# Performance work log

Measured on AMD Instinct MI355X. Metric: run time of the kernel, lower is better.

## Reference

```python
import jax, jax.numpy as jnp
import numpy as np

B, T, D, H, C = 256, 512, 64, 512, 1

def setup_inputs() -> dict:
    key = jax.random.key(0)
    ks = jax.random.split(key, 12)
    return {
        "x": jax.random.normal(ks[0], (B, T, D), jnp.float32),
        "w_ih_mu": jax.random.normal(ks[1], (D, 4 * H), jnp.float32) * 0.1,
        "w_ih_rho": jax.random.normal(ks[2], (D, 4 * H), jnp.float32) - 6.0,
        "eps_ih": jax.random.normal(ks[3], (D, 4 * H), jnp.float32),
        "w_hh_mu": jax.random.normal(ks[4], (H, 4 * H), jnp.float32) * 0.1,
        "w_hh_rho": jax.random.normal(ks[5], (H, 4 * H), jnp.float32) - 6.0,
        "eps_hh": jax.random.normal(ks[6], (H, 4 * H), jnp.float32),
        "b_mu": jax.random.normal(ks[7], (4 * H,), jnp.float32) * 0.1,
        "b_rho": jax.random.normal(ks[8], (4 * H,), jnp.float32) - 6.0,
        "eps_b": jax.random.normal(ks[9], (4 * H,), jnp.float32),
        "lin_w": jax.random.normal(ks[10], (C, H), jnp.float32) * 0.04,
        "lin_b": jax.random.normal(ks[11], (C,), jnp.float32) * 0.04,
    }

def _sample(mu, rho, eps):
    # blitz reparameterization: sigma = log1p(exp(rho))
    return mu + jnp.log1p(jnp.exp(rho)) * eps

def reference(x, w_ih_mu, w_ih_rho, eps_ih, w_hh_mu, w_hh_rho, eps_hh,
              b_mu, b_rho, eps_b, lin_w, lin_b):
    w_ih = _sample(w_ih_mu, w_ih_rho, eps_ih)
    w_hh = _sample(w_hh_mu, w_hh_rho, eps_hh)
    b = _sample(b_mu, b_rho, eps_b)

    # precompute input projections for all timesteps: [T, B, 4H]
    x_proj = jnp.einsum('btd,dg->tbg', x, w_ih) + b

    def step(carry, xp_t):
        h, c = carry
        gates = xp_t + h @ w_hh                      # [B, 4H]
        i, f, g, o = jnp.split(gates, 4, axis=-1)
        i = jax.nn.sigmoid(i)
        f = jax.nn.sigmoid(f)
        g = jnp.tanh(g)
        o = jax.nn.sigmoid(o)
        c = f * c + i * g
        h = o * jnp.tanh(c)
        return (h, c), None

    h0 = jnp.zeros((x.shape[0], w_hh.shape[0]), x.dtype)
    (h_last, _), _ = jax.lax.scan(step, (h0, h0), x_proj)
    # original takes outputs[:, -1, :] == last hidden state, then Linear
    return h_last @ lin_w.T + lin_b
```

## Files before the change

### kernel.cpp

```cpp
#include <hip/hip_runtime.h>

typedef unsigned short u16;
typedef unsigned long long u64;
typedef short v8s __attribute__((ext_vector_type(8)));
typedef float v4f __attribute__((ext_vector_type(4)));
typedef unsigned v2u __attribute__((ext_vector_type(2)));
typedef unsigned v4u __attribute__((ext_vector_type(4)));

#define Bb 256
#define Tt 512
#define Dd 64
#define Hh 512
#define G4 2048

#define NGROUP 16
#define NCHUNK 16
#define BT 16
#define HC 32
#define NCOL 128

#define WHH_S 520
#define WIH_S 72
#define SMEM_BYTES (NCOL*WHH_S*2 + NCOL*WIH_S*2)

#define MFMA(a,b,c) __builtin_amdgcn_mfma_f32_16x16x32_bf16((a),(b),(c),0,0,0)

#define SENT 0xFFFFFFFFu

__device__ __forceinline__ u16 f2bf(float f) {
  unsigned u = __float_as_uint(f);
  unsigned r = (u + 0x7fffu + ((u >> 16) & 1u)) >> 16;
  return (u16)r;
}
__device__ __forceinline__ float bf2f(u16 v) {
  return __uint_as_float(((unsigned)v) << 16);
}
__device__ __forceinline__ float sigm(float x) { return 1.0f / (1.0f + __expf(-x)); }
__device__ __forceinline__ float tanh_f(float x) {
  float a = fabsf(x);
  float e = __expf(-2.0f * a);
  float r = (1.0f - e) / (1.0f + e);
  return copysignf(r, x);
}
__device__ __forceinline__ float softplus_f(float x) { return log1pf(__expf(x)); }

__global__ void k_prep(const float* __restrict__ x, u16* __restrict__ x_bf,
                       u16* __restrict__ h_buf)
{
  int stride = gridDim.x * blockDim.x;
  int gid = blockIdx.x * blockDim.x + threadIdx.x;

  const int NS = 4 * Bb * Hh / 8;
  for (int i = gid; i < NS; i += stride)
    ((uint4*)h_buf)[i] = make_uint4(~0u, ~0u, ~0u, ~0u);

  const int N4 = Tt * Bb * Dd / 4;
  for (int i = gid; i < N4; i += stride) {
    int idx = i * 4;
    int t = idx >> 14;
    int rem = idx & 16383;
    int b = rem >> 6;
    int d = rem & 63;
    float4 v = *(const float4*)(x + (size_t)b * (Tt * Dd) + t * Dd + d);
    unsigned lo = (unsigned)f2bf(v.x) | ((unsigned)f2bf(v.y) << 16);
    unsigned hi = (unsigned)f2bf(v.z) | ((unsigned)f2bf(v.w) << 16);
    *(uint2*)(x_bf + idx) = make_uint2(lo, hi);
  }
}

__global__ __launch_bounds__(128, 1) void lstm_main(
    const float* __restrict__ whh_mu, const float* __restrict__ whh_rho, const float* __restrict__ whh_eps,
    const float* __restrict__ wih_mu, const float* __restrict__ wih_rho, const float* __restrict__ wih_eps,
    const float* __restrict__ b_mu,  const float* __restrict__ b_rho,  const float* __restrict__ b_eps,
    const u16* __restrict__ x_bf, u16* __restrict__ h_buf)
{
  extern __shared__ char smem[];
  u16* w_hh_lds = (u16*)smem;
  u16* w_ih_lds = w_hh_lds + NCOL * WHH_S;

  const int tid   = threadIdx.x;
  const int g     = blockIdx.x & 15;
  const int chunk = blockIdx.x >> 4;
  const int b0    = g * BT;
  const int j0    = chunk * HC;

  {
    const int lc = tid;
    const int gcol = (lc >> 5) * Hh + j0 + (lc & 31);
    #pragma unroll 4
    for (int k = 0; k < Hh; ++k) {
      int gi = k * G4 + gcol;
      float w = whh_mu[gi] + softplus_f(whh_rho[gi]) * whh_eps[gi];
      w_hh_lds[lc * WHH_S + k] = f2bf(w);
    }
    #pragma unroll 4
    for (int k = 0; k < Dd; ++k) {
      int gi = k * G4 + gcol;
      float w = wih_mu[gi] + softplus_f(wih_rho[gi]) * wih_eps[gi];
      w_ih_lds[lc * WIH_S + k] = f2bf(w);
    }
  }

  const int lane = tid & 63;
  const int wv   = tid >> 6;
  const int ln   = lane & 15;
  const int q    = lane >> 4;
  const int ko   = q * 8;

  const u16* WhP[4]; const u16* WxP[4];
  #pragma unroll
  for (int gt = 0; gt < 4; ++gt) {
    int rt = gt * 2 + wv;
    WhP[gt] = w_hh_lds + (rt * 16 + ln) * WHH_S + ko;
    WxP[gt] = w_ih_lds + (rt * 16 + ln) * WIH_S + ko;
  }

  const int bat = b0 + ln;

  float bs[4][4];
  #pragma unroll
  for (int gt = 0; gt < 4; ++gt)
    #pragma unroll
    for (int r = 0; r < 4; ++r) {
      int colg = gt * Hh + j0 + wv * 16 + q * 4 + r;
      bs[gt][r] = b_mu[colg] + softplus_f(b_rho[colg]) * b_eps[colg];
    }

  float cc[4] = {0.f, 0.f, 0.f, 0.f};
  __syncthreads();

  for (int t = 0; t < Tt; ++t) {
    v4f ac0 = {0.f,0.f,0.f,0.f}, ac1 = {0.f,0.f,0.f,0.f};
    v4f ac2 = {0.f,0.f,0.f,0.f}, ac3 = {0.f,0.f,0.f,0.f};

    {
      const u16* xb = x_bf + (size_t)t * (Bb * Dd) + bat * Dd + ko;
      #pragma unroll
      for (int ks = 0; ks < 2; ++ks) {
        v8s xf = *(const v8s*)(xb + ks * 32);
        ac0 = MFMA(*(const v8s*)(WxP[0] + ks * 32), xf, ac0);
        ac1 = MFMA(*(const v8s*)(WxP[1] + ks * 32), xf, ac1);
        ac2 = MFMA(*(const v8s*)(WxP[2] + ks * 32), xf, ac2);
        ac3 = MFMA(*(const v8s*)(WxP[3] + ks * 32), xf, ac3);
      }
    }

    if (t > 0) {
      const u16* hb = h_buf + (size_t)(t & 3) * (Bb * Hh) + bat * Hh + ko;
      unsigned done = 0;
      v4u buf[16];
      do {
        #pragma unroll
        for (int c = 0; c < 16; ++c)
          if (!(done & (1u << c))) {
            asm volatile("global_load_dwordx4 %0, %1, off offset:%c2 sc0 sc1"
                         : "=v"(buf[c]) : "v"(hb), "i"(c * 64));
          }
        asm volatile("s_waitcnt vmcnt(0)");
        unsigned ready = 0;
        #pragma unroll
        for (int c = 0; c < 16; ++c)
          if (!(done & (1u << c))) {
            asm volatile("" : "+v"(buf[c]));
            unsigned m0 = buf[c][0] > buf[c][1] ? buf[c][0] : buf[c][1];
            unsigned m1 = buf[c][2] > buf[c][3] ? buf[c][2] : buf[c][3];
            unsigned mx = m0 > m1 ? m0 : m1;
            int ok = (mx != SENT);
            if (__all(ok)) ready |= (1u << c);
          }
        #pragma unroll
        for (int c = 0; c < 16; ++c)
          if (ready & (1u << c)) {
            v8s hf = __builtin_bit_cast(v8s, buf[c]);
            ac0 = MFMA(*(const v8s*)(WhP[0] + c * 32), hf, ac0);
            ac1 = MFMA(*(const v8s*)(WhP[1] + c * 32), hf, ac1);
            ac2 = MFMA(*(const v8s*)(WhP[2] + c * 32), hf, ac2);
            ac3 = MFMA(*(const v8s*)(WhP[3] + c * 32), hf, ac3);
          }
        done |= ready;
      } while (done != 0xFFFFu);
    }

    {
      u16 hv[4];
      #pragma unroll
      for (int r = 0; r < 4; ++r) {
        float ig = sigm  (ac0[r] + bs[0][r]);
        float fg = sigm  (ac1[r] + bs[1][r]);
        float gg = tanh_f(ac2[r] + bs[2][r]);
        float og = sigm  (ac3[r] + bs[3][r]);
        cc[r] = fg * cc[r] + ig * gg;
        hv[r] = f2bf(og * tanh_f(cc[r]));
      }
      v2u qv;
      qv[0] = (unsigned)hv[0] | ((unsigned)hv[1] << 16);
      qv[1] = (unsigned)hv[2] | ((unsigned)hv[3] << 16);
      u16* hp = h_buf + (size_t)((t + 1) & 3) * (Bb * Hh) + bat * Hh
              + j0 + wv * 16 + q * 4;
      asm volatile("global_store_dwordx2 %0, %1, off sc0 sc1"
                   :: "v"(hp), "v"(qv) : "memory");
    }

    if (t > 0) {
      u16* cp = h_buf + (size_t)((t - 1) & 3) * (Bb * Hh) + bat * Hh
              + j0 + wv * 16 + q * 4;
      v2u sv; sv[0] = SENT; sv[1] = SENT;
      asm volatile("global_store_dwordx2 %0, %1, off sc0 sc1"
                   :: "v"(cp), "v"(sv) : "memory");
    }
  }
}

__global__ void k_out(const u16* __restrict__ h, const float* __restrict__ lw,
                      const float* __restrict__ lb, float* __restrict__ out)
{
  int b = blockIdx.x * 64 + threadIdx.x;
  if (b >= Bb) return;
  const u16* hr = h + b * Hh;
  float acc = 0.f;
  #pragma unroll 8
  for (int k = 0; k < Hh; ++k) acc += bf2f(hr[k]) * lw[k];
  out[b] = acc + lb[0];
}

extern "C" void kernel_launch(void* const* d_in, const int* in_sizes, int n_in,
                              void* d_out, int out_size, void* d_ws, size_t ws_size,
                              hipStream_t stream)
{
  (void)in_sizes; (void)n_in; (void)out_size; (void)ws_size;
  const float* x       = (const float*)d_in[0];
  const float* wih_mu  = (const float*)d_in[1];
  const float* wih_rho = (const float*)d_in[2];
  const float* wih_eps = (const float*)d_in[3];
  const float* whh_mu  = (const float*)d_in[4];
  const float* whh_rho = (const float*)d_in[5];
  const float* whh_eps = (const float*)d_in[6];
  const float* b_mu    = (const float*)d_in[7];
  const float* b_rho   = (const float*)d_in[8];
  const float* b_eps   = (const float*)d_in[9];
  const float* lin_w   = (const float*)d_in[10];
  const float* lin_b   = (const float*)d_in[11];
  float* out = (float*)d_out;

  u16* x_bf  = (u16*)d_ws;
  u16* h_buf = x_bf + (size_t)Tt * Bb * Dd;

  k_prep<<<2048, 256, 0, stream>>>(x, x_bf, h_buf);

  hipFuncSetAttribute(reinterpret_cast<const void*>(lstm_main),
                      hipFuncAttributeMaxDynamicSharedMemorySize, SMEM_BYTES);
  lstm_main<<<NGROUP * NCHUNK, 128, SMEM_BYTES, stream>>>(
      whh_mu, whh_rho, whh_eps, wih_mu, wih_rho, wih_eps,
      b_mu, b_rho, b_eps, x_bf, h_buf);

  k_out<<<(Bb + 63) / 64, 64, 0, stream>>>(h_buf, lin_w, lin_b, out);
}
```

Before: 2.500 ms.

## Use XCD-local cache scope for hidden-state exchange when group shares an XCD

Blocks record their XCC_ID in a workspace array, and each group of 16 chunks checks whether all its blocks landed on the same XCD. Blocks are also remapped to batch groups so that a group's blocks are likely to be co-located. If the whole group is on one XCD, the hidden-state exchange uses agent-scope (sc0) stores, plus an L2-level buffer_inv and plain loads while polling, with a system-scope reload every eighth spin. Otherwise it keeps the original sc0 sc1 system-coherent path. The aim is to cut the latency of per-timestep cross-block synchronization, at the risk of coherence problems if the placement assumption or cache-scope semantics are wrong.

After: 4.764 ms. 1.91x slower.

```diff
diff --git a/kernel.cpp b/kernel.cpp
--- a/kernel.cpp
+++ b/kernel.cpp
@@ -50,7 +50,7 @@
   int stride = gridDim.x * blockDim.x;
   int gid = blockIdx.x * blockDim.x + threadIdx.x;
 
-  const int NS = 4 * Bb * Hh / 8;
+  const int NS = (4 * Bb * Hh * 2 + 256 * 4) / 16;
   for (int i = gid; i < NS; i += stride)
     ((uint4*)h_buf)[i] = make_uint4(~0u, ~0u, ~0u, ~0u);
 
@@ -68,66 +68,13 @@
   }
 }
 
-__global__ __launch_bounds__(128, 1) void lstm_main(
-    const float* __restrict__ whh_mu, const float* __restrict__ whh_rho, const float* __restrict__ whh_eps,
-    const float* __restrict__ wih_mu, const float* __restrict__ wih_rho, const float* __restrict__ wih_eps,
-    const float* __restrict__ b_mu,  const float* __restrict__ b_rho,  const float* __restrict__ b_eps,
-    const u16* __restrict__ x_bf, u16* __restrict__ h_buf)
-{
-  extern __shared__ char smem[];
-  u16* w_hh_lds = (u16*)smem;
-  u16* w_ih_lds = w_hh_lds + NCOL * WHH_S;
-
-  const int tid   = threadIdx.x;
-  const int g     = blockIdx.x & 15;
-  const int chunk = blockIdx.x >> 4;
-  const int b0    = g * BT;
-  const int j0    = chunk * HC;
-
-  {
-    const int lc = tid;
-    const int gcol = (lc >> 5) * Hh + j0 + (lc & 31);
-    #pragma unroll 4
-    for (int k = 0; k < Hh; ++k) {
-      int gi = k * G4 + gcol;
-      float w = whh_mu[gi] + softplus_f(whh_rho[gi]) * whh_eps[gi];
-      w_hh_lds[lc * WHH_S + k] = f2bf(w);
-    }
-    #pragma unroll 4
-    for (int k = 0; k < Dd; ++k) {
-      int gi = k * G4 + gcol;
-      float w = wih_mu[gi] + softplus_f(wih_rho[gi]) * wih_eps[gi];
-      w_ih_lds[lc * WIH_S + k] = f2bf(w);
-    }
-  }
-
-  const int lane = tid & 63;
-  const int wv   = tid >> 6;
-  const int ln   = lane & 15;
-  const int q    = lane >> 4;
-  const int ko   = q * 8;
-
-  const u16* WhP[4]; const u16* WxP[4];
-  #pragma unroll
-  for (int gt = 0; gt < 4; ++gt) {
-    int rt = gt * 2 + wv;
-    WhP[gt] = w_hh_lds + (rt * 16 + ln) * WHH_S + ko;
-    WxP[gt] = w_ih_lds + (rt * 16 + ln) * WIH_S + ko;
-  }
-
-  const int bat = b0 + ln;
-
-  float bs[4][4];
-  #pragma unroll
-  for (int gt = 0; gt < 4; ++gt)
-    #pragma unroll
-    for (int r = 0; r < 4; ++r) {
-      int colg = gt * Hh + j0 + wv * 16 + q * 4 + r;
-      bs[gt][r] = b_mu[colg] + softplus_f(b_rho[colg]) * b_eps[colg];
-    }
-
+template<bool FAST>
+__device__ __forceinline__ void run_steps(
+    const u16* const* WhP, const u16* const* WxP,
+    const float (*bs)[4], const u16* __restrict__ x_bf,
+    u16* __restrict__ h_buf, int bat, int j0, int wv, int q, int ko)
+{
   float cc[4] = {0.f, 0.f, 0.f, 0.f};
-  __syncthreads();
 
   for (int t = 0; t < Tt; ++t) {
     v4f ac0 = {0.f,0.f,0.f,0.f}, ac1 = {0.f,0.f,0.f,0.f};
@@ -147,15 +94,26 @@
 
     if (t > 0) {
       const u16* hb = h_buf + (size_t)(t & 3) * (Bb * Hh) + bat * Hh + ko;
-      unsigned done = 0;
+      unsigned done = 0, spin = 0;
       v4u buf[16];
       do {
-        #pragma unroll
-        for (int c = 0; c < 16; ++c)
-          if (!(done & (1u << c))) {
-            asm volatile("global_load_dwordx4 %0, %1, off offset:%c2 sc0 sc1"
-                         : "=v"(buf[c]) : "v"(hb), "i"(c * 64));
-          }
+        if constexpr (FAST) {
+          asm volatile("buffer_inv sc0" ::: "memory");
+        }
+        bool sys = !FAST || ((++spin & 7u) == 7u);
+        if (sys) {
+          #pragma unroll
+          for (int c = 0; c < 16; ++c)
+            if (!(done & (1u << c)))
+              asm volatile("global_load_dwordx4 %0, %1, off offset:%c2 sc0 sc1"
+                           : "=v"(buf[c]) : "v"(hb), "i"(c * 64));
+        } else {
+          #pragma unroll
+          for (int c = 0; c < 16; ++c)
+            if (!(done & (1u << c)))
+              asm volatile("global_load_dwordx4 %0, %1, off offset:%c2"
+                           : "=v"(buf[c]) : "v"(hb), "i"(c * 64));
+        }
         asm volatile("s_waitcnt vmcnt(0)");
         unsigned ready = 0;
         #pragma unroll
@@ -197,18 +155,121 @@
       qv[1] = (unsigned)hv[2] | ((unsigned)hv[3] << 16);
       u16* hp = h_buf + (size_t)((t + 1) & 3) * (Bb * Hh) + bat * Hh
               + j0 + wv * 16 + q * 4;
-      asm volatile("global_store_dwordx2 %0, %1, off sc0 sc1"
-                   :: "v"(hp), "v"(qv) : "memory");
+      if constexpr (FAST)
+        asm volatile("global_store_dwordx2 %0, %1, off sc0"
+                     :: "v"(hp), "v"(qv) : "memory");
+      else
+        asm volatile("global_store_dwordx2 %0, %1, off sc0 sc1"
+                     :: "v"(hp), "v"(qv) : "memory");
     }
 
     if (t > 0) {
       u16* cp = h_buf + (size_t)((t - 1) & 3) * (Bb * Hh) + bat * Hh
               + j0 + wv * 16 + q * 4;
       v2u sv; sv[0] = SENT; sv[1] = SENT;
-      asm volatile("global_store_dwordx2 %0, %1, off sc0 sc1"
-                   :: "v"(cp), "v"(sv) : "memory");
-    }
-  }
+      if constexpr (FAST)
+        asm volatile("global_store_dwordx2 %0, %1, off sc0"
+                     :: "v"(cp), "v"(sv) : "memory");
+      else
+        asm volatile("global_store_dwordx2 %0, %1, off sc0 sc1"
+                     :: "v"(cp), "v"(sv) : "memory");
+    }
+  }
+}
+
+__global__ __launch_bounds__(128, 1) void lstm_main(
+    const float* __restrict__ whh_mu, const float* __restrict__ whh_rho, const float* __restrict__ whh_eps,
+    const float* __restrict__ wih_mu, const float* __restrict__ wih_rho, const float* __restrict__ wih_eps,
+    const float* __restrict__ b_mu,  const float* __restrict__ b_rho,  const float* __restrict__ b_eps,
+    const u16* __restrict__ x_bf, u16* __restrict__ h_buf)
+{
+  extern __shared__ char smem[];
+  u16* w_hh_lds = (u16*)smem;
+  u16* w_ih_lds = w_hh_lds + NCOL * WHH_S;
+
+  const int tid = threadIdx.x;
+  const int jrow  = blockIdx.x & 15;
+  const int g     = ((jrow & 7) << 1) | (jrow >> 3);
+  const int chunk = blockIdx.x >> 4;
+  const int b0    = g * BT;
+  const int j0    = chunk * HC;
+
+  unsigned* xcd_arr = (unsigned*)(h_buf + 4 * Bb * Hh);
+
+  unsigned myx;
+  asm volatile("s_getreg_b32 %0, hwreg(HW_REG_XCC_ID)" : "=s"(myx));
+  myx &= 0xffu;
+  unsigned mv = 0x100u | myx;
+  if (tid == 0) {
+    unsigned* xp = xcd_arr + blockIdx.x;
+    asm volatile("global_store_dword %0, %1, off sc0 sc1"
+                 :: "v"(xp), "v"(mv) : "memory");
+  }
+
+  {
+    const int lc = tid;
+    const int gcol = (lc >> 5) * Hh + j0 + (lc & 31);
+    #pragma unroll 4
+    for (int k = 0; k < Hh; ++k) {
+      int gi = k * G4 + gcol;
+      float w = whh_mu[gi] + softplus_f(whh_rho[gi]) * whh_eps[gi];
+      w_hh_lds[lc * WHH_S + k] = f2bf(w);
+    }
+    #pragma unroll 4
+    for (int k = 0; k < Dd; ++k) {
+      int gi = k * G4 + gcol;
+      float w = wih_mu[gi] + softplus_f(wih_rho[gi]) * wih_eps[gi];
+      w_ih_lds[lc * WIH_S + k] = f2bf(w);
+    }
+  }
+
+  const int lane = tid & 63;
+  const int wv   = tid >> 6;
+  const int ln   = lane & 15;
+  const int q    = lane >> 4;
+  const int ko   = q * 8;
+
+  const u16* WhP[4]; const u16* WxP[4];
+  #pragma unroll
+  for (int gt = 0; gt < 4; ++gt) {
+    int rt = gt * 2 + wv;
+    WhP[gt] = w_hh_lds + (rt * 16 + ln) * WHH_S + ko;
+    WxP[gt] = w_ih_lds + (rt * 16 + ln) * WIH_S + ko;
+  }
+
+  const int bat = b0 + ln;
+
+  float bs[4][4];
+  #pragma unroll
+  for (int gt = 0; gt < 4; ++gt)
+    #pragma unroll
+    for (int r = 0; r < 4; ++r) {
+      int colg = gt * Hh + j0 + wv * 16 + q * 4 + r;
+      bs[gt][r] = b_mu[colg] + softplus_f(b_rho[colg]) * b_eps[colg];
+    }
+
+  int fast;
+  {
+    const unsigned* xp = xcd_arr + (lane & 15) * 16 + jrow;
+    for (;;) {
+      unsigned v;
+      asm volatile("global_load_dword %0, %1, off sc0 sc1"
+                   : "=v"(v) : "v"(xp));
+      asm volatile("s_waitcnt vmcnt(0)");
+      asm volatile("" : "+v"(v));
+      if (__all((int)(v != SENT))) {
+        fast = __all((int)(v == mv));
+        break;
+      }
+    }
+  }
+
+  __syncthreads();
+
+  if (fast)
+    run_steps<true >(WhP, WxP, bs, x_bf, h_buf, bat, j0, wv, q, ko);
+  else
+    run_steps<false>(WhP, WxP, bs, x_bf, h_buf, bat, j0, wv, q, ko);
 }
 
 __global__ void k_out(const u16* __restrict__ h, const float* __restrict__ lw,
```
